# Kernel optimization log

Hardware: AMD Instinct MI355X
Metric: run time of the kernel (lower is better)

## Reference

```python
import jax, jax.numpy as jnp
import numpy as np

B, D, K, V = 8192, 64, 200, 100000
EPS = 1e-5


def setup_inputs() -> dict:
    key = jax.random.key(0)
    ks = jax.random.split(key, 16)
    n = lambda k, s, sc=1.0: jax.random.normal(k, s, dtype=jnp.float32) * sc
    sw = 0.05  # weight scale for numeric stability
    inp = {
        'v_embed': n(ks[0], (V, D)),
        'embeds_u_1': n(ks[1], (B, D)),
        'embeds_u_2': n(ks[2], (B, D)),
        'embeds_u_3': n(ks[3], (B, D)),
        'embeds_u_4': n(ks[4], (B, D)),
        'embeds_v': n(ks[5], (B, D)),
        'w_ur1_w': n(ks[6], (D, D), sw), 'w_ur1_b': jnp.zeros((D,), jnp.float32),
        'w_ur2_w': n(ks[7], (D, D), sw), 'w_ur2_b': jnp.zeros((D,), jnp.float32),
        'w_vr1_w': n(ks[8], (D, D), sw), 'w_vr1_b': jnp.zeros((D,), jnp.float32),
        'w_vr2_w': n(ks[9], (D, D), sw), 'w_vr2_b': jnp.zeros((D,), jnp.float32),
        'w_uv1_w': n(ks[10], (2 * D, D), sw), 'w_uv1_b': jnp.zeros((D,), jnp.float32),
        'w_uv2_w': n(ks[11], (D, 16), sw), 'w_uv2_b': jnp.zeros((16,), jnp.float32),
        'w_uv3_w': n(ks[12], (16, 1), sw), 'w_uv3_b': jnp.zeros((1,), jnp.float32),
        'nodes_v': jax.random.randint(ks[13], (B,), 0, V),
        'nbr_idx': jax.random.randint(ks[14], (B, K), 0, V),
        'nbr_len': jax.random.randint(ks[15], (B,), 1, K),
    }
    for name, dim in (('bn1', D), ('bn2', D), ('bn3', D), ('bn4', 16)):
        inp[name + '_g'] = jnp.ones((dim,), jnp.float32)
        inp[name + '_b'] = jnp.zeros((dim,), jnp.float32)
        inp[name + '_m'] = jnp.zeros((dim,), jnp.float32)
        inp[name + '_v'] = jnp.ones((dim,), jnp.float32)
    return inp


def _bn(x, g, b, m, v):
    return (x - m) * jax.lax.rsqrt(v + EPS) * g + b


def reference(v_embed, embeds_u_1, embeds_u_2, embeds_u_3, embeds_u_4, embeds_v,
              w_ur1_w, w_ur1_b, w_ur2_w, w_ur2_b,
              w_vr1_w, w_vr1_b, w_vr2_w, w_vr2_b,
              w_uv1_w, w_uv1_b, w_uv2_w, w_uv2_b, w_uv3_w, w_uv3_b,
              bn1_g, bn1_b, bn1_m, bn1_v,
              bn2_g, bn2_b, bn2_m, bn2_v,
              bn3_g, bn3_b, bn3_m, bn3_v,
              bn4_g, bn4_b, bn4_m, bn4_v,
              nodes_v, nbr_idx, nbr_len):
    sg = jax.lax.stop_gradient
    # ragged nearest-neighbor min distance (torch used .data -> detached)
    ve = sg(v_embed)
    new_v = ve[nodes_v]                                    # [B, D]
    nbr = ve[nbr_idx]                                      # [B, K, D]
    d = jnp.sqrt(jnp.sum((new_v[:, None, :] - nbr) ** 2, axis=-1))  # [B, K]
    kk = nbr_idx.shape[1]
    mask = jnp.arange(kk)[None, :] < jnp.maximum(nbr_len, 1)[:, None]
    d_min = jnp.min(jnp.where(mask, d, jnp.inf), axis=1)   # [B]
    # per-sample curiosity c_u (detached in torch via .data)
    dist = lambda a, b: jnp.sqrt(jnp.sum((a - b) ** 2, axis=-1))
    u1, u2, u3, u4 = sg(embeds_u_1), sg(embeds_u_2), sg(embeds_u_3), sg(embeds_u_4)
    c = (dist(u1, u2) + dist(u2, u3) + dist(u3, u4)) / 3.0  # [B]
    # exponential-decay fusion of temporal user embeddings: e^-4..e^-1 / sum
    w = jnp.exp(-jnp.arange(4, 0, -1, dtype=jnp.float32))
    w = w / jnp.sum(w)
    embeds_u = (embeds_u_1 * w[0] + embeds_u_2 * w[1]
                + embeds_u_3 * w[2] + embeds_u_4 * w[3])
    # MLP head (eval mode: BN with running stats, dropout off)
    x_u = jax.nn.relu(_bn(embeds_u @ w_ur1_w + w_ur1_b, bn1_g, bn1_b, bn1_m, bn1_v))
    x_u = x_u @ w_ur2_w + w_ur2_b
    x_v = jax.nn.relu(_bn(embeds_v @ w_vr1_w + w_vr1_b, bn2_g, bn2_b, bn2_m, bn2_v))
    x_v = x_v @ w_vr2_w + w_vr2_b
    x = jnp.concatenate([x_u, x_v], axis=1)                # [B, 2D]
    x = jax.nn.relu(_bn(x @ w_uv1_w + w_uv1_b, bn3_g, bn3_b, bn3_m, bn3_v))
    x = jax.nn.relu(_bn(x @ w_uv2_w + w_uv2_b, bn4_g, bn4_b, bn4_m, bn4_v))
    scores = (x @ w_uv3_w + w_uv3_b)[:, 0]                 # [B]
    # unexpectedness term: batch min-max normalize, 6t*exp(-6t)
    t = (d_min - jnp.min(d_min)) / (jnp.max(d_min) - jnp.min(d_min))
    unexp = 6.0 * t * jnp.exp(-6.0 * t)
    cn = (c - jnp.min(c)) / (jnp.max(c) - jnp.min(c))
    return scores + unexp * cn
```

## Files before the change

### kernel.cpp

```cpp
#include <hip/hip_runtime.h>
#include <math.h>

#define NROWS 8192
#define DIM 64
#define KNBR 200
#define BN_EPS 1e-5f
#define BIGF 3.402823466e38f


__device__ __forceinline__ float matvec64(const float* xlds,
                                          const float* __restrict__ W,
                                          int lane) {
    float acc = 0.f;
#pragma unroll
    for (int i4 = 0; i4 < 16; ++i4) {
        float4 xv = *(const float4*)(xlds + i4 * 4);
        acc = fmaf(xv.x, W[(i4 * 4 + 0) * 64 + lane], acc);
        acc = fmaf(xv.y, W[(i4 * 4 + 1) * 64 + lane], acc);
        acc = fmaf(xv.z, W[(i4 * 4 + 2) * 64 + lane], acc);
        acc = fmaf(xv.w, W[(i4 * 4 + 3) * 64 + lane], acc);
    }
    return acc;
}

__device__ __forceinline__ float matvec128(const float* xlds,
                                           const float* __restrict__ W,
                                           int lane) {
    float acc = 0.f;
#pragma unroll
    for (int i4 = 0; i4 < 32; ++i4) {
        float4 xv = *(const float4*)(xlds + i4 * 4);
        acc = fmaf(xv.x, W[(i4 * 4 + 0) * 64 + lane], acc);
        acc = fmaf(xv.y, W[(i4 * 4 + 1) * 64 + lane], acc);
        acc = fmaf(xv.z, W[(i4 * 4 + 2) * 64 + lane], acc);
        acc = fmaf(xv.w, W[(i4 * 4 + 3) * 64 + lane], acc);
    }
    return acc;
}

__device__ __forceinline__ float d2part(const float4 a, const float4 b) {
    const float dx = a.x - b.x, dy = a.y - b.y, dz = a.z - b.z, dw = a.w - b.w;
    float d2 = dx * dx;
    d2 = fmaf(dy, dy, d2);
    d2 = fmaf(dz, dz, d2);
    d2 = fmaf(dw, dw, d2);
    return d2;
}

__device__ __forceinline__ float sum16(float v) {
    v += __shfl_xor(v, 1);
    v += __shfl_xor(v, 2);
    v += __shfl_xor(v, 4);
    v += __shfl_xor(v, 8);
    return v;
}

__global__ __launch_bounds__(256) void fused_rows(
    const float* __restrict__ v_embed,
    const float* __restrict__ u1p, const float* __restrict__ u2p,
    const float* __restrict__ u3p, const float* __restrict__ u4p,
    const float* __restrict__ evp,
    const float* __restrict__ w_ur1, const float* __restrict__ b_ur1,
    const float* __restrict__ w_ur2, const float* __restrict__ b_ur2,
    const float* __restrict__ w_vr1, const float* __restrict__ b_vr1,
    const float* __restrict__ w_vr2, const float* __restrict__ b_vr2,
    const float* __restrict__ w_uv1, const float* __restrict__ b_uv1,
    const float* __restrict__ w_uv2, const float* __restrict__ b_uv2,
    const float* __restrict__ w_uv3, const float* __restrict__ b_uv3,
    const float* __restrict__ bn1_g, const float* __restrict__ bn1_b,
    const float* __restrict__ bn1_m, const float* __restrict__ bn1_v,
    const float* __restrict__ bn2_g, const float* __restrict__ bn2_b,
    const float* __restrict__ bn2_m, const float* __restrict__ bn2_v,
    const float* __restrict__ bn3_g, const float* __restrict__ bn3_b,
    const float* __restrict__ bn3_m, const float* __restrict__ bn3_v,
    const float* __restrict__ bn4_g, const float* __restrict__ bn4_b,
    const float* __restrict__ bn4_m, const float* __restrict__ bn4_v,
    const int* __restrict__ nodes_v, const int* __restrict__ nbr_idx,
    const int* __restrict__ nbr_len,
    float* __restrict__ out_score, float* __restrict__ ws_d2,
    float* __restrict__ ws_c) {
    const int w = threadIdx.x >> 6;
    const int lane = threadIdx.x & 63;
    const int row = blockIdx.x * 4 + w;

    __shared__ float xbuf[4][132];
    float* xw = xbuf[w];

    const size_t rb = (size_t)row * DIM + lane;
    const float u1 = u1p[rb], u2 = u2p[rb], u3 = u3p[rb], u4 = u4p[rb];
    const float ev = evp[rb];

    float d12 = u1 - u2, d23 = u2 - u3, d34 = u3 - u4;
    float s1 = d12 * d12, s2 = d23 * d23, s3 = d34 * d34;
#pragma unroll
    for (int m = 1; m < 64; m <<= 1) {
        s1 += __shfl_xor(s1, m);
        s2 += __shfl_xor(s2, m);
        s3 += __shfl_xor(s3, m);
    }
    const float cval = (sqrtf(s1) + sqrtf(s2) + sqrtf(s3)) * (1.0f / 3.0f);

    float eu = u1 * 0.032058603280084993f;
    eu = fmaf(u2, 0.087144318742032567f, eu);
    eu = fmaf(u3, 0.236882818089910134f, eu);
    eu = fmaf(u4, 0.643914259887972245f, eu);

    xw[lane] = eu;
    float t1 = matvec64(xw, w_ur1, lane) + b_ur1[lane];
    t1 = (t1 - bn1_m[lane]) * rsqrtf(bn1_v[lane] + BN_EPS) * bn1_g[lane] + bn1_b[lane];
    t1 = fmaxf(t1, 0.f);
    xw[lane] = t1;
    const float xu = matvec64(xw, w_ur2, lane) + b_ur2[lane];
    xw[lane] = ev;
    float t2 = matvec64(xw, w_vr1, lane) + b_vr1[lane];
    t2 = (t2 - bn2_m[lane]) * rsqrtf(bn2_v[lane] + BN_EPS) * bn2_g[lane] + bn2_b[lane];
    t2 = fmaxf(t2, 0.f);
    xw[lane] = t2;
    const float xv = matvec64(xw, w_vr2, lane) + b_vr2[lane];
    xw[lane] = xu;
    xw[64 + lane] = xv;
    float t3 = matvec128(xw, w_uv1, lane) + b_uv1[lane];
    t3 = (t3 - bn3_m[lane]) * rsqrtf(bn3_v[lane] + BN_EPS) * bn3_g[lane] + bn3_b[lane];
    t3 = fmaxf(t3, 0.f);
    xw[lane] = t3;
    const int j = lane & 15;
    const int q = lane >> 4;
    float h4 = 0.f;
#pragma unroll
    for (int i = 0; i < 16; ++i) {
        h4 = fmaf(xw[q * 16 + i], w_uv2[(q * 16 + i) * 16 + j], h4);
    }
    h4 += __shfl_xor(h4, 16);
    h4 += __shfl_xor(h4, 32);
    h4 += b_uv2[j];
    h4 = (h4 - bn4_m[j]) * rsqrtf(bn4_v[j] + BN_EPS) * bn4_g[j] + bn4_b[j];
    h4 = fmaxf(h4, 0.f);
    float p = h4 * w_uv3[j];
#pragma unroll
    for (int m = 1; m < 16; m <<= 1) p += __shfl_xor(p, m);
    const float score = p + b_uv3[0];

    const int node = nodes_v[row];
    const int l16 = lane & 15;
    const float4 vq = ((const float4*)(v_embed + ((size_t)node << 6)))[l16];
    int len = nbr_len[row];
    if (len < 1) len = 1;
    const int* nb = nbr_idx + (size_t)row * KNBR;
    const int myoff = lane >> 4;
    float dmin2 = BIGF;
    for (int k0 = 0; k0 < len; k0 += 16) {
        const int ka = k0 + myoff;
        const int kb = k0 + 4 + myoff;
        const int kc = k0 + 8 + myoff;
        const int kd = k0 + 12 + myoff;
        const bool va = ka < len, vb = kb < len, vc = kc < len, vd = kd < len;
        const int ia = nb[va ? ka : 0];
        const int ib = nb[vb ? kb : 0];
        const int ic = nb[vc ? kc : 0];
        const int id = nb[vd ? kd : 0];
        const float4 na = ((const float4*)(v_embed + ((size_t)ia << 6)))[l16];
        const float4 nbv = ((const float4*)(v_embed + ((size_t)ib << 6)))[l16];
        const float4 nc = ((const float4*)(v_embed + ((size_t)ic << 6)))[l16];
        const float4 nd = ((const float4*)(v_embed + ((size_t)id << 6)))[l16];
        float da = sum16(d2part(vq, na));
        float db = sum16(d2part(vq, nbv));
        float dc = sum16(d2part(vq, nc));
        float dd = sum16(d2part(vq, nd));
        dmin2 = fminf(dmin2, va ? da : BIGF);
        dmin2 = fminf(dmin2, vb ? db : BIGF);
        dmin2 = fminf(dmin2, vc ? dc : BIGF);
        dmin2 = fminf(dmin2, vd ? dd : BIGF);
    }
    dmin2 = fminf(dmin2, __shfl_xor(dmin2, 16));
    dmin2 = fminf(dmin2, __shfl_xor(dmin2, 32));

    if (lane == 0) {
        out_score[row] = score;
        ws_d2[row] = dmin2;
        ws_c[row] = cval;
    }
}

__global__ __launch_bounds__(1024) void combine(
    const float* __restrict__ ws_d2, const float* __restrict__ ws_c,
    float* __restrict__ out) {
    const int tid = threadIdx.x;
    __shared__ float red[4][16];

    float ld2[8], lc[8];
    float dmin = BIGF, dmax = -BIGF, cmin = BIGF, cmax = -BIGF;
#pragma unroll
    for (int i = 0; i < 8; ++i) {
        const int b = tid * 8 + i;
        ld2[i] = ws_d2[b];
        lc[i] = ws_c[b];
        dmin = fminf(dmin, ld2[i]);
        dmax = fmaxf(dmax, ld2[i]);
        cmin = fminf(cmin, lc[i]);
        cmax = fmaxf(cmax, lc[i]);
    }
#pragma unroll
    for (int m = 1; m < 64; m <<= 1) {
        dmin = fminf(dmin, __shfl_xor(dmin, m));
        dmax = fmaxf(dmax, __shfl_xor(dmax, m));
        cmin = fminf(cmin, __shfl_xor(cmin, m));
        cmax = fmaxf(cmax, __shfl_xor(cmax, m));
    }
    const int wid = tid >> 6;
    const int lane = tid & 63;
    if (lane == 0) {
        red[0][wid] = dmin;
        red[1][wid] = dmax;
        red[2][wid] = cmin;
        red[3][wid] = cmax;
    }
    __syncthreads();
    dmin = red[0][0]; dmax = red[1][0]; cmin = red[2][0]; cmax = red[3][0];
#pragma unroll
    for (int i = 1; i < 16; ++i) {
        dmin = fminf(dmin, red[0][i]);
        dmax = fmaxf(dmax, red[1][i]);
        cmin = fminf(cmin, red[2][i]);
        cmax = fmaxf(cmax, red[3][i]);
    }
    const float dlo = sqrtf(dmin);
    const float dhi = sqrtf(dmax);
    const float inv_d = 1.f / (dhi - dlo);
    const float inv_c = 1.f / (cmax - cmin);
#pragma unroll
    for (int i = 0; i < 8; ++i) {
        const int b = tid * 8 + i;
        const float t = (sqrtf(ld2[i]) - dlo) * inv_d;
        const float unexp = 6.f * t * expf(-6.f * t);
        out[b] += unexp * (lc[i] - cmin) * inv_c;
    }
}

extern "C" void kernel_launch(void* const* d_in, const int* in_sizes, int n_in,
                              void* d_out, int out_size, void* d_ws, size_t ws_size,
                              hipStream_t stream) {
    const float* v_embed = (const float*)d_in[0];
    const float* u1 = (const float*)d_in[1];
    const float* u2 = (const float*)d_in[2];
    const float* u3 = (const float*)d_in[3];
    const float* u4 = (const float*)d_in[4];
    const float* ev = (const float*)d_in[5];
    const float* w_ur1 = (const float*)d_in[6];
    const float* b_ur1 = (const float*)d_in[7];
    const float* w_ur2 = (const float*)d_in[8];
    const float* b_ur2 = (const float*)d_in[9];
    const float* w_vr1 = (const float*)d_in[10];
    const float* b_vr1 = (const float*)d_in[11];
    const float* w_vr2 = (const float*)d_in[12];
    const float* b_vr2 = (const float*)d_in[13];
    const float* w_uv1 = (const float*)d_in[14];
    const float* b_uv1 = (const float*)d_in[15];
    const float* w_uv2 = (const float*)d_in[16];
    const float* b_uv2 = (const float*)d_in[17];
    const float* w_uv3 = (const float*)d_in[18];
    const float* b_uv3 = (const float*)d_in[19];
    const int* nodes_v = (const int*)d_in[20];
    const int* nbr_idx = (const int*)d_in[21];
    const int* nbr_len = (const int*)d_in[22];
    const float* bn1_g = (const float*)d_in[23];
    const float* bn1_b = (const float*)d_in[24];
    const float* bn1_m = (const float*)d_in[25];
    const float* bn1_v = (const float*)d_in[26];
    const float* bn2_g = (const float*)d_in[27];
    const float* bn2_b = (const float*)d_in[28];
    const float* bn2_m = (const float*)d_in[29];
    const float* bn2_v = (const float*)d_in[30];
    const float* bn3_g = (const float*)d_in[31];
    const float* bn3_b = (const float*)d_in[32];
    const float* bn3_m = (const float*)d_in[33];
    const float* bn3_v = (const float*)d_in[34];
    const float* bn4_g = (const float*)d_in[35];
    const float* bn4_b = (const float*)d_in[36];
    const float* bn4_m = (const float*)d_in[37];
    const float* bn4_v = (const float*)d_in[38];

    float* out = (float*)d_out;
    float* wsf = (float*)d_ws;
    float* ws_d2 = wsf;
    float* ws_c = wsf + NROWS;

    hipLaunchKernelGGL(fused_rows, dim3(NROWS / 4), dim3(256), 0, stream,
                       v_embed, u1, u2, u3, u4, ev,
                       w_ur1, b_ur1, w_ur2, b_ur2, w_vr1, b_vr1, w_vr2, b_vr2,
                       w_uv1, b_uv1, w_uv2, b_uv2, w_uv3, b_uv3,
                       bn1_g, bn1_b, bn1_m, bn1_v,
                       bn2_g, bn2_b, bn2_m, bn2_v,
                       bn3_g, bn3_b, bn3_m, bn3_v,
                       bn4_g, bn4_b, bn4_m, bn4_v,
                       nodes_v, nbr_idx, nbr_len,
                       out, ws_d2, ws_c);
    hipLaunchKernelGGL(combine, dim3(1), dim3(1024), 0, stream,
                       ws_d2, ws_c, out);
}
```

Before: 62.85 us.

## Split each row's neighbor scan across all eight waves of a block

The block grows to 512 threads covering 8 rows. All eight waves now work together on every row's ragged nearest-neighbor scan, with each wave taking a strided subset of the neighbors. Per-wave partial minima go into shared memory and are combined after a block barrier. This evens out the load imbalance from variable neighbor lengths, which in the old code left one wave looping for up to 200 neighbors. In exchange it adds a __syncthreads and predicated iterations for short rows, and the launch bounds now request higher occupancy.

```diff
diff --git a/kernel.cpp b/kernel.cpp
--- a/kernel.cpp
+++ b/kernel.cpp
@@ -55,7 +55,7 @@
     return v;
 }
 
-__global__ __launch_bounds__(256) void fused_rows(
+__global__ __launch_bounds__(512, 8) void fused_rows(
     const float* __restrict__ v_embed,
     const float* __restrict__ u1p, const float* __restrict__ u2p,
     const float* __restrict__ u3p, const float* __restrict__ u4p,
@@ -81,12 +81,50 @@
     float* __restrict__ ws_c) {
     const int w = threadIdx.x >> 6;
     const int lane = threadIdx.x & 63;
-    const int row = blockIdx.x * 4 + w;
-
-    __shared__ float xbuf[4][132];
+    const int row0 = blockIdx.x * 8;
+    const int myrow = row0 + w;
+
+    __shared__ float xbuf[8][132];
+    __shared__ float pmins[8][9];
+
+    const int l16 = lane & 15;
+    const int g = lane >> 4;
+
+#pragma unroll 2
+    for (int r = 0; r < 8; ++r) {
+        const int row = row0 + r;
+        const int node = nodes_v[row];
+        const float4 vq = ((const float4*)(v_embed + ((size_t)node << 6)))[l16];
+        int len = nbr_len[row];
+        if (len < 1) len = 1;
+        const int* nb = nbr_idx + (size_t)row * KNBR;
+        float dmin2 = BIGF;
+#pragma unroll
+        for (int j = 0; j < 4; ++j) {
+            if (len > w + 64 * j) {
+                const int sA = 8 * j + g;
+                const int sB = 8 * j + 4 + g;
+                const int kA = w + 8 * sA;
+                const int kB = w + 8 * sB;
+                const int kAc = kA < len ? kA : (len - 1);
+                const int kBc = kB < len ? kB : (len - 1);
+                const int iA = nb[kAc];
+                const int iB = nb[kBc];
+                const float4 nA = ((const float4*)(v_embed + ((size_t)iA << 6)))[l16];
+                const float4 nB = ((const float4*)(v_embed + ((size_t)iB << 6)))[l16];
+                const float dA = sum16(d2part(vq, nA));
+                const float dB = sum16(d2part(vq, nB));
+                dmin2 = fminf(dmin2, kA < len ? dA : BIGF);
+                dmin2 = fminf(dmin2, kB < len ? dB : BIGF);
+            }
+        }
+        dmin2 = fminf(dmin2, __shfl_xor(dmin2, 16));
+        dmin2 = fminf(dmin2, __shfl_xor(dmin2, 32));
+        if (lane == 0) pmins[r][w] = dmin2;
+    }
+
     float* xw = xbuf[w];
-
-    const size_t rb = (size_t)row * DIM + lane;
+    const size_t rb = (size_t)myrow * DIM + lane;
     const float u1 = u1p[rb], u2 = u2p[rb], u3 = u3p[rb], u4 = u4p[rb];
     const float ev = evp[rb];
 
@@ -123,61 +161,36 @@
     t3 = (t3 - bn3_m[lane]) * rsqrtf(bn3_v[lane] + BN_EPS) * bn3_g[lane] + bn3_b[lane];
     t3 = fmaxf(t3, 0.f);
     xw[lane] = t3;
-    const int j = lane & 15;
+    const int jj = lane & 15;
     const int q = lane >> 4;
     float h4 = 0.f;
 #pragma unroll
     for (int i = 0; i < 16; ++i) {
-        h4 = fmaf(xw[q * 16 + i], w_uv2[(q * 16 + i) * 16 + j], h4);
+        h4 = fmaf(xw[q * 16 + i], w_uv2[(q * 16 + i) * 16 + jj], h4);
     }
     h4 += __shfl_xor(h4, 16);
     h4 += __shfl_xor(h4, 32);
-    h4 += b_uv2[j];
-    h4 = (h4 - bn4_m[j]) * rsqrtf(bn4_v[j] + BN_EPS) * bn4_g[j] + bn4_b[j];
+    h4 += b_uv2[jj];
+    h4 = (h4 - bn4_m[jj]) * rsqrtf(bn4_v[jj] + BN_EPS) * bn4_g[jj] + bn4_b[jj];
     h4 = fmaxf(h4, 0.f);
-    float p = h4 * w_uv3[j];
+    float p = h4 * w_uv3[jj];
 #pragma unroll
     for (int m = 1; m < 16; m <<= 1) p += __shfl_xor(p, m);
     const float score = p + b_uv3[0];
 
-    const int node = nodes_v[row];
-    const int l16 = lane & 15;
-    const float4 vq = ((const float4*)(v_embed + ((size_t)node << 6)))[l16];
-    int len = nbr_len[row];
-    if (len < 1) len = 1;
-    const int* nb = nbr_idx + (size_t)row * KNBR;
-    const int myoff = lane >> 4;
-    float dmin2 = BIGF;
-    for (int k0 = 0; k0 < len; k0 += 16) {
-        const int ka = k0 + myoff;
-        const int kb = k0 + 4 + myoff;
-        const int kc = k0 + 8 + myoff;
-        const int kd = k0 + 12 + myoff;
-        const bool va = ka < len, vb = kb < len, vc = kc < len, vd = kd < len;
-        const int ia = nb[va ? ka : 0];
-        const int ib = nb[vb ? kb : 0];
-        const int ic = nb[vc ? kc : 0];
-        const int id = nb[vd ? kd : 0];
-        const float4 na = ((const float4*)(v_embed + ((size_t)ia << 6)))[l16];
-        const float4 nbv = ((const float4*)(v_embed + ((size_t)ib << 6)))[l16];
-        const float4 nc = ((const float4*)(v_embed + ((size_t)ic << 6)))[l16];
-        const float4 nd = ((const float4*)(v_embed + ((size_t)id << 6)))[l16];
-        float da = sum16(d2part(vq, na));
-        float db = sum16(d2part(vq, nbv));
-        float dc = sum16(d2part(vq, nc));
-        float dd = sum16(d2part(vq, nd));
-        dmin2 = fminf(dmin2, va ? da : BIGF);
-        dmin2 = fminf(dmin2, vb ? db : BIGF);
-        dmin2 = fminf(dmin2, vc ? dc : BIGF);
-        dmin2 = fminf(dmin2, vd ? dd : BIGF);
-    }
-    dmin2 = fminf(dmin2, __shfl_xor(dmin2, 16));
-    dmin2 = fminf(dmin2, __shfl_xor(dmin2, 32));
-
     if (lane == 0) {
-        out_score[row] = score;
-        ws_d2[row] = dmin2;
-        ws_c[row] = cval;
+        out_score[myrow] = score;
+        ws_c[myrow] = cval;
+    }
+
+    __syncthreads();
+    if (w == 0) {
+        const int r = lane >> 3;
+        float v = pmins[r][lane & 7];
+        v = fminf(v, __shfl_xor(v, 1));
+        v = fminf(v, __shfl_xor(v, 2));
+        v = fminf(v, __shfl_xor(v, 4));
+        if ((lane & 7) == 0) ws_d2[row0 + r] = v;
     }
 }
 
@@ -284,7 +297,7 @@
     float* ws_d2 = wsf;
     float* ws_c = wsf + NROWS;
 
-    hipLaunchKernelGGL(fused_rows, dim3(NROWS / 4), dim3(256), 0, stream,
+    hipLaunchKernelGGL(fused_rows, dim3(NROWS / 8), dim3(512), 0, stream,
                        v_embed, u1, u2, u3, u4, ev,
                        w_ur1, b_ur1, w_ur2, b_ur2, w_vr1, b_vr1, w_vr2, b_vr2,
                        w_uv1, b_uv1, w_uv2, b_uv2, w_uv3, b_uv3,
```

After: 122.7 us. +95.2%, slower.

## Split neighbor min-distance search into per-chunk blocks with partial minima

Applied to the files above, without the earlier changes.

The neighbor scan is split across a second grid dimension: seven phases each handle 32 neighbors per row and write partial minima to a workspace, while an eighth phase runs the MLP head. The combine kernel reduces the partial minima per row using nbr_len before the global min/max normalization. This exposes more parallel memory-latency hiding for the gather-bound search, in exchange for a larger workspace, an extra query-vector load per chunk, and more reduction work in the single-block combine.

```diff
diff --git a/kernel.cpp b/kernel.cpp
--- a/kernel.cpp
+++ b/kernel.cpp
@@ -4,6 +4,7 @@
 #define NROWS 8192
 #define DIM 64
 #define KNBR 200
+#define NCHUNK 7
 #define BN_EPS 1e-5f
 #define BIGF 3.402823466e38f
 
@@ -55,7 +56,7 @@
     return v;
 }
 
-__global__ __launch_bounds__(256) void fused_rows(
+__global__ __launch_bounds__(256) void fused_main(
     const float* __restrict__ v_embed,
     const float* __restrict__ u1p, const float* __restrict__ u2p,
     const float* __restrict__ u3p, const float* __restrict__ u4p,
@@ -77,15 +78,76 @@
     const float* __restrict__ bn4_m, const float* __restrict__ bn4_v,
     const int* __restrict__ nodes_v, const int* __restrict__ nbr_idx,
     const int* __restrict__ nbr_len,
-    float* __restrict__ out_score, float* __restrict__ ws_d2,
+    float* __restrict__ out_score, float* __restrict__ part,
     float* __restrict__ ws_c) {
     const int w = threadIdx.x >> 6;
     const int lane = threadIdx.x & 63;
     const int row = blockIdx.x * 4 + w;
+    const int phase = blockIdx.y;
 
     __shared__ float xbuf[4][132];
+
+    if (phase < NCHUNK) {
+        int len = nbr_len[row];
+        if (len < 1) len = 1;
+        const int k0 = phase * 32;
+        if (k0 >= len) return;
+
+        const int l16 = lane & 15;
+        const int g = lane >> 4;
+        const int node = nodes_v[row];
+        const float4 vq = ((const float4*)(v_embed + ((size_t)node << 6)))[l16];
+        const int* nb = nbr_idx + (size_t)row * KNBR;
+        float dmin2 = BIGF;
+
+        {
+            const int ka = k0 + g, kb = k0 + 4 + g, kc = k0 + 8 + g, kd = k0 + 12 + g;
+            const bool va = ka < len, vb = kb < len, vc = kc < len, vd = kd < len;
+            const int ia = nb[va ? ka : 0];
+            const int ib = nb[vb ? kb : 0];
+            const int ic = nb[vc ? kc : 0];
+            const int id = nb[vd ? kd : 0];
+            const float4 na = ((const float4*)(v_embed + ((size_t)ia << 6)))[l16];
+            const float4 nbv = ((const float4*)(v_embed + ((size_t)ib << 6)))[l16];
+            const float4 nc = ((const float4*)(v_embed + ((size_t)ic << 6)))[l16];
+            const float4 nd = ((const float4*)(v_embed + ((size_t)id << 6)))[l16];
+            const float da = sum16(d2part(vq, na));
+            const float db = sum16(d2part(vq, nbv));
+            const float dc = sum16(d2part(vq, nc));
+            const float dd = sum16(d2part(vq, nd));
+            dmin2 = fminf(dmin2, va ? da : BIGF);
+            dmin2 = fminf(dmin2, vb ? db : BIGF);
+            dmin2 = fminf(dmin2, vc ? dc : BIGF);
+            dmin2 = fminf(dmin2, vd ? dd : BIGF);
+        }
+        if (k0 + 16 < len) {
+            const int k1 = k0 + 16;
+            const int ka = k1 + g, kb = k1 + 4 + g, kc = k1 + 8 + g, kd = k1 + 12 + g;
+            const bool va = ka < len, vb = kb < len, vc = kc < len, vd = kd < len;
+            const int ia = nb[va ? ka : 0];
+            const int ib = nb[vb ? kb : 0];
+            const int ic = nb[vc ? kc : 0];
+            const int id = nb[vd ? kd : 0];
+            const float4 na = ((const float4*)(v_embed + ((size_t)ia << 6)))[l16];
+            const float4 nbv = ((const float4*)(v_embed + ((size_t)ib << 6)))[l16];
+            const float4 nc = ((const float4*)(v_embed + ((size_t)ic << 6)))[l16];
+            const float4 nd = ((const float4*)(v_embed + ((size_t)id << 6)))[l16];
+            const float da = sum16(d2part(vq, na));
+            const float db = sum16(d2part(vq, nbv));
+            const float dc = sum16(d2part(vq, nc));
+            const float dd = sum16(d2part(vq, nd));
+            dmin2 = fminf(dmin2, va ? da : BIGF);
+            dmin2 = fminf(dmin2, vb ? db : BIGF);
+            dmin2 = fminf(dmin2, vc ? dc : BIGF);
+            dmin2 = fminf(dmin2, vd ? dd : BIGF);
+        }
+        dmin2 = fminf(dmin2, __shfl_xor(dmin2, 16));
+        dmin2 = fminf(dmin2, __shfl_xor(dmin2, 32));
+        if (lane == 0) part[row * NCHUNK + phase] = dmin2;
+        return;
+    }
+
     float* xw = xbuf[w];
-
     const size_t rb = (size_t)row * DIM + lane;
     const float u1 = u1p[rb], u2 = u2p[rb], u3 = u3p[rb], u4 = u4p[rb];
     const float ev = evp[rb];
@@ -123,67 +185,32 @@
     t3 = (t3 - bn3_m[lane]) * rsqrtf(bn3_v[lane] + BN_EPS) * bn3_g[lane] + bn3_b[lane];
     t3 = fmaxf(t3, 0.f);
     xw[lane] = t3;
-    const int j = lane & 15;
+    const int jj = lane & 15;
     const int q = lane >> 4;
     float h4 = 0.f;
 #pragma unroll
     for (int i = 0; i < 16; ++i) {
-        h4 = fmaf(xw[q * 16 + i], w_uv2[(q * 16 + i) * 16 + j], h4);
+        h4 = fmaf(xw[q * 16 + i], w_uv2[(q * 16 + i) * 16 + jj], h4);
     }
     h4 += __shfl_xor(h4, 16);
     h4 += __shfl_xor(h4, 32);
-    h4 += b_uv2[j];
-    h4 = (h4 - bn4_m[j]) * rsqrtf(bn4_v[j] + BN_EPS) * bn4_g[j] + bn4_b[j];
+    h4 += b_uv2[jj];
+    h4 = (h4 - bn4_m[jj]) * rsqrtf(bn4_v[jj] + BN_EPS) * bn4_g[jj] + bn4_b[jj];
     h4 = fmaxf(h4, 0.f);
-    float p = h4 * w_uv3[j];
+    float p = h4 * w_uv3[jj];
 #pragma unroll
     for (int m = 1; m < 16; m <<= 1) p += __shfl_xor(p, m);
     const float score = p + b_uv3[0];
 
-    const int node = nodes_v[row];
-    const int l16 = lane & 15;
-    const float4 vq = ((const float4*)(v_embed + ((size_t)node << 6)))[l16];
-    int len = nbr_len[row];
-    if (len < 1) len = 1;
-    const int* nb = nbr_idx + (size_t)row * KNBR;
-    const int myoff = lane >> 4;
-    float dmin2 = BIGF;
-    for (int k0 = 0; k0 < len; k0 += 16) {
-        const int ka = k0 + myoff;
-        const int kb = k0 + 4 + myoff;
-        const int kc = k0 + 8 + myoff;
-        const int kd = k0 + 12 + myoff;
-        const bool va = ka < len, vb = kb < len, vc = kc < len, vd = kd < len;
-        const int ia = nb[va ? ka : 0];
-        const int ib = nb[vb ? kb : 0];
-        const int ic = nb[vc ? kc : 0];
-        const int id = nb[vd ? kd : 0];
-        const float4 na = ((const float4*)(v_embed + ((size_t)ia << 6)))[l16];
-        const float4 nbv = ((const float4*)(v_embed + ((size_t)ib << 6)))[l16];
-        const float4 nc = ((const float4*)(v_embed + ((size_t)ic << 6)))[l16];
-        const float4 nd = ((const float4*)(v_embed + ((size_t)id << 6)))[l16];
-        float da = sum16(d2part(vq, na));
-        float db = sum16(d2part(vq, nbv));
-        float dc = sum16(d2part(vq, nc));
-        float dd = sum16(d2part(vq, nd));
-        dmin2 = fminf(dmin2, va ? da : BIGF);
-        dmin2 = fminf(dmin2, vb ? db : BIGF);
-        dmin2 = fminf(dmin2, vc ? dc : BIGF);
-        dmin2 = fminf(dmin2, vd ? dd : BIGF);
-    }
-    dmin2 = fminf(dmin2, __shfl_xor(dmin2, 16));
-    dmin2 = fminf(dmin2, __shfl_xor(dmin2, 32));
-
     if (lane == 0) {
         out_score[row] = score;
-        ws_d2[row] = dmin2;
         ws_c[row] = cval;
     }
 }
 
 __global__ __launch_bounds__(1024) void combine(
-    const float* __restrict__ ws_d2, const float* __restrict__ ws_c,
-    float* __restrict__ out) {
+    const float* __restrict__ part, const float* __restrict__ ws_c,
+    const int* __restrict__ nbr_len, float* __restrict__ out) {
     const int tid = threadIdx.x;
     __shared__ float red[4][16];
 
@@ -192,10 +219,15 @@
 #pragma unroll
     for (int i = 0; i < 8; ++i) {
         const int b = tid * 8 + i;
-        ld2[i] = ws_d2[b];
+        int len = nbr_len[b];
+        if (len < 1) len = 1;
+        const int nch = (len + 31) >> 5;
+        float m = part[b * NCHUNK];
+        for (int c = 1; c < nch; ++c) m = fminf(m, part[b * NCHUNK + c]);
+        ld2[i] = m;
         lc[i] = ws_c[b];
-        dmin = fminf(dmin, ld2[i]);
-        dmax = fmaxf(dmax, ld2[i]);
+        dmin = fminf(dmin, m);
+        dmax = fmaxf(dmax, m);
         cmin = fminf(cmin, lc[i]);
         cmax = fmaxf(cmax, lc[i]);
     }
@@ -281,10 +313,10 @@
 
     float* out = (float*)d_out;
     float* wsf = (float*)d_ws;
-    float* ws_d2 = wsf;
-    float* ws_c = wsf + NROWS;
-
-    hipLaunchKernelGGL(fused_rows, dim3(NROWS / 4), dim3(256), 0, stream,
+    float* part = wsf;
+    float* ws_c = wsf + NROWS * NCHUNK;
+
+    hipLaunchKernelGGL(fused_main, dim3(NROWS / 4, 8), dim3(256), 0, stream,
                        v_embed, u1, u2, u3, u4, ev,
                        w_ur1, b_ur1, w_ur2, b_ur2, w_vr1, b_vr1, w_vr2, b_vr2,
                        w_uv1, b_uv1, w_uv2, b_uv2, w_uv3, b_uv3,
@@ -293,7 +325,7 @@
                        bn3_g, bn3_b, bn3_m, bn3_v,
                        bn4_g, bn4_b, bn4_m, bn4_v,
                        nodes_v, nbr_idx, nbr_len,
-                       out, ws_d2, ws_c);
+                       out, part, ws_c);
     hipLaunchKernelGGL(combine, dim3(1), dim3(1024), 0, stream,
-                       ws_d2, ws_c, out);
-}
+                       part, ws_c, nbr_len, out);
+}
```

Measured after the change: 87.54 us. 39.3% more time.

## Assign one neighbor per lane in nearest-neighbor distance loop

Applied to the files above, without the earlier changes.

Restructures the ragged neighbor min-distance search so each lane processes a whole neighbor row instead of 16 lanes cooperating on one row with shuffle reductions. The query vector is staged in shared memory and the distance loop is moved ahead of the MLP head. This removes per-neighbor cross-lane shuffles and reduces loop iterations, at the cost of uncoalesced per-lane row gathers that may hurt memory efficiency.

```diff
diff --git a/kernel.cpp b/kernel.cpp
--- a/kernel.cpp
+++ b/kernel.cpp
@@ -36,23 +36,6 @@
         acc = fmaf(xv.w, W[(i4 * 4 + 3) * 64 + lane], acc);
     }
     return acc;
-}
-
-__device__ __forceinline__ float d2part(const float4 a, const float4 b) {
-    const float dx = a.x - b.x, dy = a.y - b.y, dz = a.z - b.z, dw = a.w - b.w;
-    float d2 = dx * dx;
-    d2 = fmaf(dy, dy, d2);
-    d2 = fmaf(dz, dz, d2);
-    d2 = fmaf(dw, dw, d2);
-    return d2;
-}
-
-__device__ __forceinline__ float sum16(float v) {
-    v += __shfl_xor(v, 1);
-    v += __shfl_xor(v, 2);
-    v += __shfl_xor(v, 4);
-    v += __shfl_xor(v, 8);
-    return v;
 }
 
 __global__ __launch_bounds__(256) void fused_rows(
@@ -84,8 +67,62 @@
     const int row = blockIdx.x * 4 + w;
 
     __shared__ float xbuf[4][132];
+    __shared__ float qbuf[4][64];
+
+    const int node = nodes_v[row];
+    const float* vrow = v_embed + ((size_t)node << 6);
+    if (lane < 16) {
+        const float4 vq = ((const float4*)vrow)[lane];
+        *(float4*)&qbuf[w][lane * 4] = vq;
+    }
+    __syncthreads();
+
+    int len = nbr_len[row];
+    if (len < 1) len = 1;
+    const int* nb = nbr_idx + (size_t)row * KNBR;
+
+    float dmin2 = BIGF;
+    for (int k0 = 0; k0 < len; k0 += 64) {
+        int k = k0 + lane;
+        if (k >= len) k = len - 1;
+        const int idx = nb[k];
+        const float4* np4 = (const float4*)(v_embed + ((size_t)idx << 6));
+        float a0 = 0.f, a1 = 0.f, a2 = 0.f, a3 = 0.f;
+#pragma unroll
+        for (int d4 = 0; d4 < 16; d4 += 4) {
+            const float4 n0 = np4[d4 + 0];
+            const float4 n1 = np4[d4 + 1];
+            const float4 n2 = np4[d4 + 2];
+            const float4 n3 = np4[d4 + 3];
+            const float4 q0 = *(const float4*)&qbuf[w][(d4 + 0) * 4];
+            const float4 q1 = *(const float4*)&qbuf[w][(d4 + 1) * 4];
+            const float4 q2 = *(const float4*)&qbuf[w][(d4 + 2) * 4];
+            const float4 q3 = *(const float4*)&qbuf[w][(d4 + 3) * 4];
+            float dx;
+            dx = q0.x - n0.x; a0 = fmaf(dx, dx, a0);
+            dx = q0.y - n0.y; a0 = fmaf(dx, dx, a0);
+            dx = q0.z - n0.z; a0 = fmaf(dx, dx, a0);
+            dx = q0.w - n0.w; a0 = fmaf(dx, dx, a0);
+            dx = q1.x - n1.x; a1 = fmaf(dx, dx, a1);
+            dx = q1.y - n1.y; a1 = fmaf(dx, dx, a1);
+            dx = q1.z - n1.z; a1 = fmaf(dx, dx, a1);
+            dx = q1.w - n1.w; a1 = fmaf(dx, dx, a1);
+            dx = q2.x - n2.x; a2 = fmaf(dx, dx, a2);
+            dx = q2.y - n2.y; a2 = fmaf(dx, dx, a2);
+            dx = q2.z - n2.z; a2 = fmaf(dx, dx, a2);
+            dx = q2.w - n2.w; a2 = fmaf(dx, dx, a2);
+            dx = q3.x - n3.x; a3 = fmaf(dx, dx, a3);
+            dx = q3.y - n3.y; a3 = fmaf(dx, dx, a3);
+            dx = q3.z - n3.z; a3 = fmaf(dx, dx, a3);
+            dx = q3.w - n3.w; a3 = fmaf(dx, dx, a3);
+        }
+        const float d2 = (a0 + a1) + (a2 + a3);
+        dmin2 = fminf(dmin2, d2);
+    }
+#pragma unroll
+    for (int m = 1; m < 64; m <<= 1) dmin2 = fminf(dmin2, __shfl_xor(dmin2, m));
+
     float* xw = xbuf[w];
-
     const size_t rb = (size_t)row * DIM + lane;
     const float u1 = u1p[rb], u2 = u2p[rb], u3 = u3p[rb], u4 = u4p[rb];
     const float ev = evp[rb];
@@ -123,56 +160,22 @@
     t3 = (t3 - bn3_m[lane]) * rsqrtf(bn3_v[lane] + BN_EPS) * bn3_g[lane] + bn3_b[lane];
     t3 = fmaxf(t3, 0.f);
     xw[lane] = t3;
-    const int j = lane & 15;
+    const int jj = lane & 15;
     const int q = lane >> 4;
     float h4 = 0.f;
 #pragma unroll
     for (int i = 0; i < 16; ++i) {
-        h4 = fmaf(xw[q * 16 + i], w_uv2[(q * 16 + i) * 16 + j], h4);
+        h4 = fmaf(xw[q * 16 + i], w_uv2[(q * 16 + i) * 16 + jj], h4);
     }
     h4 += __shfl_xor(h4, 16);
     h4 += __shfl_xor(h4, 32);
-    h4 += b_uv2[j];
-    h4 = (h4 - bn4_m[j]) * rsqrtf(bn4_v[j] + BN_EPS) * bn4_g[j] + bn4_b[j];
+    h4 += b_uv2[jj];
+    h4 = (h4 - bn4_m[jj]) * rsqrtf(bn4_v[jj] + BN_EPS) * bn4_g[jj] + bn4_b[jj];
     h4 = fmaxf(h4, 0.f);
-    float p = h4 * w_uv3[j];
+    float p = h4 * w_uv3[jj];
 #pragma unroll
     for (int m = 1; m < 16; m <<= 1) p += __shfl_xor(p, m);
     const float score = p + b_uv3[0];
-
-    const int node = nodes_v[row];
-    const int l16 = lane & 15;
-    const float4 vq = ((const float4*)(v_embed + ((size_t)node << 6)))[l16];
-    int len = nbr_len[row];
-    if (len < 1) len = 1;
-    const int* nb = nbr_idx + (size_t)row * KNBR;
-    const int myoff = lane >> 4;
-    float dmin2 = BIGF;
-    for (int k0 = 0; k0 < len; k0 += 16) {
-        const int ka = k0 + myoff;
-        const int kb = k0 + 4 + myoff;
-        const int kc = k0 + 8 + myoff;
-        const int kd = k0 + 12 + myoff;
-        const bool va = ka < len, vb = kb < len, vc = kc < len, vd = kd < len;
-        const int ia = nb[va ? ka : 0];
-        const int ib = nb[vb ? kb : 0];
-        const int ic = nb[vc ? kc : 0];
-        const int id = nb[vd ? kd : 0];
-        const float4 na = ((const float4*)(v_embed + ((size_t)ia << 6)))[l16];
-        const float4 nbv = ((const float4*)(v_embed + ((size_t)ib << 6)))[l16];
-        const float4 nc = ((const float4*)(v_embed + ((size_t)ic << 6)))[l16];
-        const float4 nd = ((const float4*)(v_embed + ((size_t)id << 6)))[l16];
-        float da = sum16(d2part(vq, na));
-        float db = sum16(d2part(vq, nbv));
-        float dc = sum16(d2part(vq, nc));
-        float dd = sum16(d2part(vq, nd));
-        dmin2 = fminf(dmin2, va ? da : BIGF);
-        dmin2 = fminf(dmin2, vb ? db : BIGF);
-        dmin2 = fminf(dmin2, vc ? dc : BIGF);
-        dmin2 = fminf(dmin2, vd ? dd : BIGF);
-    }
-    dmin2 = fminf(dmin2, __shfl_xor(dmin2, 16));
-    dmin2 = fminf(dmin2, __shfl_xor(dmin2, 32));
 
     if (lane == 0) {
         out_score[row] = score;
```

New measurement: 78.93 us. +25.6%, slower.
